# Optimization experiments

Measured on AMD Instinct MI355X. Metric: run time of the kernel, lower is better.

## Reference

```python
import jax, jax.numpy as jnp
import numpy as np

N_NODES = 100000
N_EDGES = 1600000
IN_F, HID_F, OUT_F = 128, 128, 64


def setup_inputs() -> dict:
    key = jax.random.key(0)
    ks = jax.random.split(key, 8)
    x = jax.random.normal(ks[0], (N_NODES, IN_F), dtype=jnp.float32)
    edge_index = jax.random.randint(ks[1], (2, N_EDGES), 0, N_NODES, dtype=jnp.int64)
    w1 = jax.random.normal(ks[2], (IN_F, HID_F), dtype=jnp.float32) * 0.05
    b1 = jax.random.normal(ks[3], (HID_F,), dtype=jnp.float32) * 0.05
    c1 = jax.random.normal(ks[4], (IN_F, HID_F, 3), dtype=jnp.float32) * 0.01
    w2 = jax.random.normal(ks[5], (HID_F, OUT_F), dtype=jnp.float32) * 0.05
    b2 = jax.random.normal(ks[6], (OUT_F,), dtype=jnp.float32) * 0.05
    c2 = jax.random.normal(ks[7], (IN_F, OUT_F, 3), dtype=jnp.float32) * 0.01
    return {"x": x, "edge_index": edge_index, "w1": w1, "b1": b1, "c1": c1,
            "w2": w2, "b2": b2, "c2": c2}


def _minimal_kan(x, w, b, c):
    # linear term: (N, out)
    lin = x @ w + b
    # polynomial basis (x, x^2, x^3): (N, in, 3)
    basis = jnp.stack([x, x * x, x * x * x], axis=-1)
    # fused contraction over (in, 3); same math as the (N,in,out,3) broadcast-sum
    kan_out = jnp.einsum('nib,iob->no', basis, c)
    return lin + 0.1 * kan_out


def _aggregate(h, source, target, num_nodes):
    # mean over incoming messages, degree clamped at 1
    deg = jax.ops.segment_sum(jnp.ones(source.shape[0], dtype=h.dtype), target,
                              num_segments=num_nodes)
    deg = jnp.maximum(deg, 1.0)
    out = jax.ops.segment_sum(h[source], target, num_segments=num_nodes)
    return out / deg[:, None]


def reference(x, edge_index, w1, b1, c1, w2, b2, c2):
    source, target = edge_index[0], edge_index[1]
    n = x.shape[0]
    h = _minimal_kan(x, w1, b1, c1)
    h = jax.nn.relu(h)
    h = _aggregate(h, source, target, n)
    h = _minimal_kan(h, w2, b2, c2)
    h = _aggregate(h, source, target, n)
    return jax.nn.log_softmax(h, axis=-1)
```

## Files before the change

### kernel.cpp

```cpp
#include <hip/hip_runtime.h>
#include <hip/hip_bf16.h>
#include <math.h>

#define N_NODES 100000
#define N_EDGES 1600000
#define IN_F 128
#define HID_F 128
#define OUT_F 64
#define K_TOT 384
#define BST 392

#define BK_BITS 9
#define BK_SIZE 512
#define NBUCK ((N_NODES + BK_SIZE - 1) / BK_SIZE)
#define EPB 4096
#define NBLK_SORT ((N_EDGES + EPB - 1) / EPB)
#define BCAP 10240
#define PCAP (BCAP + 7 * BK_SIZE)
#define PK_SRC_MASK 0x7fffffu
#define PAD8(d) (((d) + 7) & ~7)

typedef __attribute__((ext_vector_type(8))) short s8v;
typedef __attribute__((ext_vector_type(4))) short s4v;
typedef __attribute__((ext_vector_type(4))) float f4v;
typedef __attribute__((ext_vector_type(2))) float f2v;

__device__ __forceinline__ short f2bf(float f) {
    __hip_bfloat16 h = __float2bfloat16(f);
    return __builtin_bit_cast(short, h);
}

__global__ __launch_bounds__(256) void fold_weights_bf16(
    const float* __restrict__ w1, const float* __restrict__ c1,
    const float* __restrict__ w2, const float* __restrict__ c2,
    short* __restrict__ Wb1, short* __restrict__ Wb2,
    unsigned* __restrict__ h1d, unsigned* __restrict__ h2d,
    int* __restrict__ bcur)
{
    if (blockIdx.x == 0) {
        if (threadIdx.x < 32) h1d[(size_t)N_NODES * 32 + threadIdx.x] = 0;
        if (threadIdx.x < 16) h2d[(size_t)N_NODES * 16 + threadIdx.x] = 0;
        if (threadIdx.x < NBUCK) bcur[threadIdx.x] = threadIdx.x * BCAP;
    }
    int idx = blockIdx.x * 256 + threadIdx.x;
    if (idx < K_TOT * HID_F) {
        int k = idx >> 7, n = idx & 127;
        int p = k >> 7, f = k & 127;
        int si = f * HID_F + n;
        float v = (p == 0) ? (w1[si] + 0.1f * c1[si * 3])
                           : 0.1f * c1[si * 3 + p];
        Wb1[(((k >> 3) * HID_F) + n) * 8 + (k & 7)] = f2bf(v);
    } else {
        idx -= K_TOT * HID_F;
        if (idx < K_TOT * OUT_F) {
            int k = idx >> 6, n = idx & 63;
            int p = k >> 7, f = k & 127;
            int si = f * OUT_F + n;
            float v = (p == 0) ? (w2[si] + 0.1f * c2[si * 3])
                               : 0.1f * c2[si * 3 + p];
            Wb2[(((k >> 3) * OUT_F) + n) * 8 + (k & 7)] = f2bf(v);
        }
    }
}

__global__ __launch_bounds__(256) void scatter_kan1(
    const int* __restrict__ src, const int* __restrict__ tgt,
    int* __restrict__ bcur, unsigned* __restrict__ spk,
    const float* __restrict__ x, const short* __restrict__ Wb,
    const float* __restrict__ bias, unsigned* __restrict__ h1d)
{
    __shared__ __align__(16) char smem[64 * BST * 2];
    const int tid = threadIdx.x;

    if (blockIdx.x < NBLK_SORT) {
        int* h    = (int*)smem;
        int* base = h + NBUCK;
        int* tg   = base + NBUCK;
        for (int i = tid; i < NBUCK; i += 256) h[i] = 0;
        __syncthreads();
        int e0 = blockIdx.x * EPB;
        int n = min(EPB, N_EDGES - e0);
        for (int i = tid; i < n; i += 256) {
            int t = tgt[e0 + i];
            tg[i] = t;
            atomicAdd(&h[t >> BK_BITS], 1);
        }
        __syncthreads();
        for (int i = tid; i < NBUCK; i += 256) {
            int c = h[i];
            base[i] = c ? atomicAdd(&bcur[i], c) : 0;
            h[i] = 0;
        }
        __syncthreads();
        for (int i = tid; i < n; i += 256) {
            int t = tg[i];
            int b = t >> BK_BITS;
            int pos = base[b] + atomicAdd(&h[b], 1);
            spk[pos] = ((unsigned)(t - (b << BK_BITS)) << 23) | (unsigned)src[e0 + i];
        }
        return;
    }

    short* sb = (short*)smem;
    const int lane = tid & 63;
    const int wave = tid >> 6;
    const int node0 = (blockIdx.x - NBLK_SORT) * 64;
    const int q = lane >> 4, r = lane & 15;

#pragma unroll
    for (int it = 0; it < 8; ++it) {
        int idx = tid + 256 * it;
        int m = idx >> 5, c4 = (idx & 31) * 4;
        int gm = min(node0 + m, N_NODES - 1);
        float4 v = *(const float4*)(x + (size_t)gm * IN_F + c4);
        float vv[4] = {v.x, v.y, v.z, v.w};
        s4v p0, p1, p2;
#pragma unroll
        for (int t = 0; t < 4; ++t) {
            float e = vv[t], e2 = e * e, e3 = e2 * e;
            p0[t] = f2bf(e); p1[t] = f2bf(e2); p2[t] = f2bf(e3);
        }
        short* row = sb + m * BST + c4;
        *(s4v*)(row)       = p0;
        *(s4v*)(row + 128) = p1;
        *(s4v*)(row + 256) = p2;
    }
    __syncthreads();

    const int wm = (wave & 1) * 32;
    const int wn = (wave >> 1) * 64;

    f4v acc[2][4];
#pragma unroll
    for (int i = 0; i < 2; ++i)
#pragma unroll
        for (int j = 0; j < 4; ++j)
            acc[i][j] = (f4v){0.f, 0.f, 0.f, 0.f};

    float bj[4];
#pragma unroll
    for (int j = 0; j < 4; ++j) bj[j] = bias[wn + j * 16 + r];

#pragma unroll
    for (int kb = 0; kb < 12; ++kb) {
        const int col = kb * 32 + q * 8;
        s8v afrag[2];
#pragma unroll
        for (int i = 0; i < 2; ++i)
            afrag[i] = *(const s8v*)(sb + (wm + i * 16 + r) * BST + col);
#pragma unroll
        for (int j = 0; j < 4; ++j) {
            const s8v b = *(const s8v*)(Wb + (((kb * 4 + q) * HID_F) + wn + j * 16 + r) * 8);
            acc[0][j] = __builtin_amdgcn_mfma_f32_16x16x32_bf16(afrag[0], b, acc[0][j], 0, 0, 0);
            acc[1][j] = __builtin_amdgcn_mfma_f32_16x16x32_bf16(afrag[1], b, acc[1][j], 0, 0, 0);
        }
    }

    const int dci = ((wn >> 6) << 4) + r;
#pragma unroll
    for (int i = 0; i < 2; ++i)
#pragma unroll
        for (int e = 0; e < 4; ++e) {
            int grow = node0 + wm + i * 16 + q * 4 + e;
            if (grow < N_NODES) {
                float v0 = fmaxf(acc[i][0][e] + bj[0], 0.f);
                float v1 = fmaxf(acc[i][1][e] + bj[1], 0.f);
                float v2 = fmaxf(acc[i][2][e] + bj[2], 0.f);
                float v3 = fmaxf(acc[i][3][e] + bj[3], 0.f);
                int pk = __builtin_amdgcn_cvt_pk_fp8_f32(v0, v1, 0, false);
                pk = __builtin_amdgcn_cvt_pk_fp8_f32(v2, v3, pk, true);
                h1d[(size_t)grow * 32 + dci] = (unsigned)pk;
            }
        }
}

__global__ __launch_bounds__(512) void csr_build(
    const int* __restrict__ bcur, const unsigned* __restrict__ spk,
    int* __restrict__ deg, int* __restrict__ prow, int* __restrict__ csr_pad)
{
    __shared__ int d[BK_SIZE];
    __shared__ int pst[BK_SIZE];
    __shared__ int s[BK_SIZE];
    int tid = threadIdx.x;
    int b = blockIdx.x;
    d[tid] = 0;
    __syncthreads();
    int e0 = b * BCAP, e1 = bcur[b];
    for (int i = e0 + tid; i < e1; i += 512)
        atomicAdd(&d[spk[i] >> 23], 1);
    __syncthreads();
    int nbase = b << BK_BITS;
    int node = nbase + tid;
    int a = d[tid];
    if (node < N_NODES) deg[node] = a;
    int pc = (node < N_NODES) ? PAD8(a) : 0;
    s[tid] = pc;
    __syncthreads();
    for (int o = 1; o < 512; o <<= 1) {
        int t = (tid >= o) ? s[tid - o] : 0;
        __syncthreads();
        s[tid] += t;
        __syncthreads();
    }
    int excl = s[tid] - pc;
    int base = b * PCAP + excl;
    if (node < N_NODES) prow[node] = base;
    __syncthreads();
    d[tid] = base;
    pst[tid] = base + pc;
    __syncthreads();
    for (int i = e0 + tid; i < e1; i += 512) {
        unsigned pk = spk[i];
        int pos = atomicAdd(&d[pk >> 23], 1);
        csr_pad[pos] = (int)(pk & PK_SRC_MASK);
    }
    __syncthreads();
    {
        int kend = pst[tid];
        for (int k = d[tid]; k < kend; ++k) csr_pad[k] = N_NODES;
    }
}

__global__ __launch_bounds__(256) void gather128(
    const unsigned* __restrict__ h1d, const int* __restrict__ prow,
    const int* __restrict__ deg, const int* __restrict__ csr_pad,
    unsigned* __restrict__ a1d)
{
    const int lane  = threadIdx.x & 63;
    const int wave  = threadIdx.x >> 6;
    const int hl    = lane & 31;
    const int half  = lane >> 5;
    const int hbase = half << 5;
    const int node  = blockIdx.x * 8 + wave * 2 + half;

    int p0 = prow[node];
    int cnt = PAD8(deg[node]);
    int p1 = p0 + cnt;
    int cmax = max(cnt, __shfl_xor(cnt, 32));

    float acc[4][4];
#pragma unroll
    for (int t = 0; t < 4; ++t)
#pragma unroll
        for (int b = 0; b < 4; ++b) acc[t][b] = 0.f;

    for (int base = 0; base < cmax; base += 32) {
        int idx = max(min(p0 + base + hl, p1 - 1), 0);
        int sreg = csr_pad[idx];
        int lim = min(32, cmax - base);
        for (int j = 0; j < lim; j += 4) {
            if (base + j < cnt) {
                unsigned u[4];
#pragma unroll
                for (int t = 0; t < 4; ++t) {
                    int sj = __shfl(sreg, hbase + j + t);
                    u[t] = h1d[(size_t)sj * 32 + hl];
                }
#pragma unroll
                for (int t = 0; t < 4; ++t) {
                    f2v lo = __builtin_amdgcn_cvt_pk_f32_fp8(u[t], false);
                    f2v hi = __builtin_amdgcn_cvt_pk_f32_fp8(u[t], true);
                    acc[t][0] += lo.x; acc[t][1] += lo.y;
                    acc[t][2] += hi.x; acc[t][3] += hi.y;
                }
            }
        }
    }

    float s0 = (acc[0][0] + acc[1][0]) + (acc[2][0] + acc[3][0]);
    float s1 = (acc[0][1] + acc[1][1]) + (acc[2][1] + acc[3][1]);
    float s2 = (acc[0][2] + acc[1][2]) + (acc[2][2] + acc[3][2]);
    float s3 = (acc[0][3] + acc[1][3]) + (acc[2][3] + acc[3][3]);
    int pk = __builtin_amdgcn_cvt_pk_fp8_f32(s0, s1, 0, false);
    pk = __builtin_amdgcn_cvt_pk_fp8_f32(s2, s3, pk, true);
    a1d[(size_t)node * 32 + hl] = (unsigned)pk;
}

__global__ __launch_bounds__(256) void kan2_mfma(
    const unsigned* __restrict__ a1d, const int* __restrict__ deg,
    const short* __restrict__ Wb, const float* __restrict__ bias,
    unsigned short* __restrict__ h2s)
{
    __shared__ short sb[64 * BST];
    const int tid  = threadIdx.x;
    const int lane = tid & 63;
    const int wave = tid >> 6;
    const int node0 = blockIdx.x * 64;
    const int q = lane >> 4, r = lane & 15;

#pragma unroll
    for (int gi = 0; gi < 2; ++gi) {
        int g = tid + 256 * gi;
        int m = g >> 3, cg = (g & 7) * 4;
        int gm = min(node0 + m, N_NODES - 1);
        float di = 1.0f / fmaxf((float)deg[gm], 1.0f);
        uint4 u4 = *(const uint4*)(a1d + (size_t)gm * 32 + cg);
        unsigned uw[4] = {u4.x, u4.y, u4.z, u4.w};
        float xv[4][4];
#pragma unroll
        for (int j = 0; j < 4; ++j) {
            f2v lo = __builtin_amdgcn_cvt_pk_f32_fp8(uw[j], false);
            f2v hi = __builtin_amdgcn_cvt_pk_f32_fp8(uw[j], true);
            xv[j][0] = lo.x * di; xv[j][1] = lo.y * di;
            xv[j][2] = hi.x * di; xv[j][3] = hi.y * di;
        }
        int fb = ((cg >> 4) << 6) + (cg & 15);
#pragma unroll
        for (int b = 0; b < 4; ++b) {
            s4v p0, p1, p2;
#pragma unroll
            for (int j = 0; j < 4; ++j) {
                float e = xv[j][b], e2 = e * e, e3 = e2 * e;
                p0[j] = f2bf(e); p1[j] = f2bf(e2); p2[j] = f2bf(e3);
            }
            short* row = sb + m * BST + fb + 16 * b;
            *(s4v*)(row)       = p0;
            *(s4v*)(row + 128) = p1;
            *(s4v*)(row + 256) = p2;
        }
    }
    __syncthreads();

    const int wm = (wave & 1) * 32;
    const int wn = (wave >> 1) * 32;

    f4v acc[2][2];
#pragma unroll
    for (int i = 0; i < 2; ++i)
#pragma unroll
        for (int j = 0; j < 2; ++j)
            acc[i][j] = (f4v){0.f, 0.f, 0.f, 0.f};

    float bj[2];
#pragma unroll
    for (int j = 0; j < 2; ++j) bj[j] = bias[wn + j * 16 + r];

#pragma unroll
    for (int kb = 0; kb < 12; ++kb) {
        const int col = kb * 32 + q * 8;
        s8v afrag[2];
#pragma unroll
        for (int i = 0; i < 2; ++i)
            afrag[i] = *(const s8v*)(sb + (wm + i * 16 + r) * BST + col);
#pragma unroll
        for (int j = 0; j < 2; ++j) {
            const s8v b = *(const s8v*)(Wb + (((kb * 4 + q) * OUT_F) + wn + j * 16 + r) * 8);
            acc[0][j] = __builtin_amdgcn_mfma_f32_16x16x32_bf16(afrag[0], b, acc[0][j], 0, 0, 0);
            acc[1][j] = __builtin_amdgcn_mfma_f32_16x16x32_bf16(afrag[1], b, acc[1][j], 0, 0, 0);
        }
    }

    const int sslot = (wn >> 1) + r;
#pragma unroll
    for (int i = 0; i < 2; ++i)
#pragma unroll
        for (int e = 0; e < 4; ++e) {
            int grow = node0 + wm + i * 16 + q * 4 + e;
            if (grow < N_NODES) {
                float vlo = acc[i][0][e] + bj[0];
                float vhi = acc[i][1][e] + bj[1];
                int pk = __builtin_amdgcn_cvt_pk_fp8_f32(vlo, vhi, 0, false);
                h2s[(size_t)grow * 32 + sslot] = (unsigned short)(pk & 0xffff);
            }
        }
}

__global__ __launch_bounds__(256) void gather64_lsm(
    const unsigned short* __restrict__ h2s, const int* __restrict__ deg,
    const int* __restrict__ prow, const int* __restrict__ csr_pad,
    float* __restrict__ out)
{
    const int lane = threadIdx.x & 63;
    const int wave = threadIdx.x >> 6;
    const int hl   = lane & 31;
    const int half = lane >> 5;
    const int node = blockIdx.x * 8 + wave * 2 + half;

    int p0 = prow[node];
    int degr = deg[node];
    int cnt = PAD8(degr);
    int p1 = p0 + cnt;
    int cmax = max(cnt, __shfl_xor(cnt, 32));

    float alo[8], ahi[8];
#pragma unroll
    for (int t = 0; t < 8; ++t) { alo[t] = 0.f; ahi[t] = 0.f; }

    for (int base = 0; base < cmax; base += 32) {
        int idx = max(min(p0 + base + hl, p1 - 1), 0);
        int sreg = csr_pad[idx];
        int lim = min(32, cmax - base);
        for (int j = 0; j < lim; j += 8) {
            if (base + j < cnt) {
                int u[8];
#pragma unroll
                for (int t = 0; t < 8; ++t) {
                    int sj = __shfl(sreg, (half << 5) + j + t);
                    u[t] = (int)h2s[(size_t)sj * 32 + hl];
                }
#pragma unroll
                for (int t = 0; t < 8; ++t) {
                    alo[t] += __builtin_amdgcn_cvt_f32_fp8(u[t], 0);
                    ahi[t] += __builtin_amdgcn_cvt_f32_fp8(u[t], 1);
                }
            }
        }
    }
    float slo = ((alo[0] + alo[1]) + (alo[2] + alo[3])) + ((alo[4] + alo[5]) + (alo[6] + alo[7]));
    float shi = ((ahi[0] + ahi[1]) + (ahi[2] + ahi[3])) + ((ahi[4] + ahi[5]) + (ahi[6] + ahi[7]));

    float di = 1.0f / fmaxf((float)degr, 1.0f);
    float vlo = slo * di, vhi = shi * di;

    float m = fmaxf(vlo, vhi);
#pragma unroll
    for (int off = 16; off >= 1; off >>= 1)
        m = fmaxf(m, __shfl_xor(m, off));
    float e = expf(vlo - m) + expf(vhi - m);
#pragma unroll
    for (int off = 16; off >= 1; off >>= 1)
        e += __shfl_xor(e, off);
    float ls = logf(e);

    const int f_lo = ((hl >> 4) << 5) + (hl & 15);
    out[(size_t)node * OUT_F + f_lo]      = vlo - m - ls;
    out[(size_t)node * OUT_F + f_lo + 16] = vhi - m - ls;
}

extern "C" void kernel_launch(void* const* d_in, const int* in_sizes, int n_in,
                              void* d_out, int out_size, void* d_ws, size_t ws_size,
                              hipStream_t stream)
{
    const float* x  = (const float*)d_in[0];
    const int*   ei = (const int*)d_in[1];
    const float* w1 = (const float*)d_in[2];
    const float* b1 = (const float*)d_in[3];
    const float* c1 = (const float*)d_in[4];
    const float* w2 = (const float*)d_in[5];
    const float* b2 = (const float*)d_in[6];
    const float* c2 = (const float*)d_in[7];
    float* out = (float*)d_out;

    const int* src = ei;
    const int* tgt = ei + N_EDGES;

    char* ws = (char*)d_ws;
    size_t off = 0;
    auto carve = [&](size_t bytes) -> void* {
        void* p = ws + off;
        off = (off + bytes + 255) & ~(size_t)255;
        return p;
    };
    short*    Wb1       = (short*)carve((size_t)K_TOT * HID_F * 2);
    short*    Wb2       = (short*)carve((size_t)K_TOT * OUT_F * 2);
    int*      deg       = (int*)carve((size_t)N_NODES * 4);
    int*      prow      = (int*)carve((size_t)N_NODES * 4);
    int*      bcur      = (int*)carve((size_t)NBUCK * 4);
    unsigned* spk       = (unsigned*)carve((size_t)NBUCK * BCAP * 4);
    int*      csr_pad   = (int*)carve((size_t)NBUCK * PCAP * 4);
    unsigned* h1d       = (unsigned*)carve(((size_t)N_NODES + 1) * 128);
    unsigned* a1d       = (unsigned*)carve((size_t)N_NODES * 128);
    unsigned short* h2s = (unsigned short*)carve(((size_t)N_NODES + 1) * 64);

    const int grid_mm = (N_NODES + 63) / 64;

    fold_weights_bf16<<<(K_TOT * HID_F + K_TOT * OUT_F + 255) / 256, 256, 0, stream>>>(
        w1, c1, w2, c2, Wb1, Wb2, h1d, (unsigned*)h2s, bcur);

    scatter_kan1<<<NBLK_SORT + grid_mm, 256, 0, stream>>>(
        src, tgt, bcur, spk, x, Wb1, b1, h1d);

    csr_build<<<NBUCK, 512, 0, stream>>>(bcur, spk, deg, prow, csr_pad);

    gather128<<<(N_NODES + 7) / 8, 256, 0, stream>>>(h1d, prow, deg, csr_pad, a1d);

    kan2_mfma<<<grid_mm, 256, 0, stream>>>(a1d, deg, Wb2, b2, h2s);

    gather64_lsm<<<(N_NODES + 7) / 8, 256, 0, stream>>>(
        h2s, deg, prow, csr_pad, out);
}
```

Measured before the change: 231.2 us.

## Split KAN1 GEMM blocks across scatter and CSR-build launches to overlap phases

Moves the first KAN layer's per-node GEMM into a device function and splits its tiles between the edge-scatter kernel (first 781 tiles) and a merged CSR-build kernel (the remaining tiles). The idea is to fill idle compute during the latency-bound CSR build with independent matmul work. Buckets shrink from 512 to 256 nodes so the CSR build runs with 256-thread blocks and more blocks, which changes the packed key layout (24-bit source, 8-bit local index). This adds register and shared-memory pressure to the CSR kernel and relies on a fixed split constant.

```diff
diff --git a/kernel.cpp b/kernel.cpp
--- a/kernel.cpp
+++ b/kernel.cpp
@@ -10,15 +10,19 @@
 #define K_TOT 384
 #define BST 392
 
-#define BK_BITS 9
-#define BK_SIZE 512
+#define BK_BITS 8
+#define BK_SIZE 256
 #define NBUCK ((N_NODES + BK_SIZE - 1) / BK_SIZE)
 #define EPB 4096
 #define NBLK_SORT ((N_EDGES + EPB - 1) / EPB)
-#define BCAP 10240
+#define BCAP 5120
 #define PCAP (BCAP + 7 * BK_SIZE)
-#define PK_SRC_MASK 0x7fffffu
+#define PK_SRC_MASK 0xffffffu
 #define PAD8(d) (((d) + 7) & ~7)
+
+#define K1T ((N_NODES + 63) / 64)
+#define K1A 781
+#define K1B (K1T - K1A)
 
 typedef __attribute__((ext_vector_type(8))) short s8v;
 typedef __attribute__((ext_vector_type(4))) short s4v;
@@ -40,7 +44,7 @@
     if (blockIdx.x == 0) {
         if (threadIdx.x < 32) h1d[(size_t)N_NODES * 32 + threadIdx.x] = 0;
         if (threadIdx.x < 16) h2d[(size_t)N_NODES * 16 + threadIdx.x] = 0;
-        if (threadIdx.x < NBUCK) bcur[threadIdx.x] = threadIdx.x * BCAP;
+        for (int i = threadIdx.x; i < NBUCK; i += 256) bcur[i] = i * BCAP;
     }
     int idx = blockIdx.x * 256 + threadIdx.x;
     if (idx < K_TOT * HID_F) {
@@ -63,48 +67,14 @@
     }
 }
 
-__global__ __launch_bounds__(256) void scatter_kan1(
-    const int* __restrict__ src, const int* __restrict__ tgt,
-    int* __restrict__ bcur, unsigned* __restrict__ spk,
+__device__ __forceinline__ void kan1_body(
+    short* sb, int node0,
     const float* __restrict__ x, const short* __restrict__ Wb,
     const float* __restrict__ bias, unsigned* __restrict__ h1d)
 {
-    __shared__ __align__(16) char smem[64 * BST * 2];
-    const int tid = threadIdx.x;
-
-    if (blockIdx.x < NBLK_SORT) {
-        int* h    = (int*)smem;
-        int* base = h + NBUCK;
-        int* tg   = base + NBUCK;
-        for (int i = tid; i < NBUCK; i += 256) h[i] = 0;
-        __syncthreads();
-        int e0 = blockIdx.x * EPB;
-        int n = min(EPB, N_EDGES - e0);
-        for (int i = tid; i < n; i += 256) {
-            int t = tgt[e0 + i];
-            tg[i] = t;
-            atomicAdd(&h[t >> BK_BITS], 1);
-        }
-        __syncthreads();
-        for (int i = tid; i < NBUCK; i += 256) {
-            int c = h[i];
-            base[i] = c ? atomicAdd(&bcur[i], c) : 0;
-            h[i] = 0;
-        }
-        __syncthreads();
-        for (int i = tid; i < n; i += 256) {
-            int t = tg[i];
-            int b = t >> BK_BITS;
-            int pos = base[b] + atomicAdd(&h[b], 1);
-            spk[pos] = ((unsigned)(t - (b << BK_BITS)) << 23) | (unsigned)src[e0 + i];
-        }
-        return;
-    }
-
-    short* sb = (short*)smem;
+    const int tid  = threadIdx.x;
     const int lane = tid & 63;
     const int wave = tid >> 6;
-    const int node0 = (blockIdx.x - NBLK_SORT) * 64;
     const int q = lane >> 4, r = lane & 15;
 
 #pragma unroll
@@ -174,51 +144,101 @@
         }
 }
 
-__global__ __launch_bounds__(512) void csr_build(
+__global__ __launch_bounds__(256) void scatter_kan1(
+    const int* __restrict__ src, const int* __restrict__ tgt,
+    int* __restrict__ bcur, unsigned* __restrict__ spk,
+    const float* __restrict__ x, const short* __restrict__ Wb,
+    const float* __restrict__ bias, unsigned* __restrict__ h1d)
+{
+    __shared__ __align__(16) char smem[64 * BST * 2];
+    const int tid = threadIdx.x;
+
+    if (blockIdx.x < NBLK_SORT) {
+        int* h    = (int*)smem;
+        int* base = h + NBUCK;
+        int* tg   = base + NBUCK;
+        for (int i = tid; i < NBUCK; i += 256) h[i] = 0;
+        __syncthreads();
+        int e0 = blockIdx.x * EPB;
+        int n = min(EPB, N_EDGES - e0);
+        for (int i = tid; i < n; i += 256) {
+            int t = tgt[e0 + i];
+            tg[i] = t;
+            atomicAdd(&h[t >> BK_BITS], 1);
+        }
+        __syncthreads();
+        for (int i = tid; i < NBUCK; i += 256) {
+            int c = h[i];
+            base[i] = c ? atomicAdd(&bcur[i], c) : 0;
+            h[i] = 0;
+        }
+        __syncthreads();
+        for (int i = tid; i < n; i += 256) {
+            int t = tg[i];
+            int b = t >> BK_BITS;
+            int pos = base[b] + atomicAdd(&h[b], 1);
+            spk[pos] = ((unsigned)(t - (b << BK_BITS)) << 24) | (unsigned)src[e0 + i];
+        }
+        return;
+    }
+
+    kan1_body((short*)smem, ((int)blockIdx.x - NBLK_SORT) * 64, x, Wb, bias, h1d);
+}
+
+__global__ __launch_bounds__(256) void csr_kan1(
     const int* __restrict__ bcur, const unsigned* __restrict__ spk,
-    int* __restrict__ deg, int* __restrict__ prow, int* __restrict__ csr_pad)
-{
-    __shared__ int d[BK_SIZE];
-    __shared__ int pst[BK_SIZE];
-    __shared__ int s[BK_SIZE];
-    int tid = threadIdx.x;
-    int b = blockIdx.x;
-    d[tid] = 0;
-    __syncthreads();
-    int e0 = b * BCAP, e1 = bcur[b];
-    for (int i = e0 + tid; i < e1; i += 512)
-        atomicAdd(&d[spk[i] >> 23], 1);
-    __syncthreads();
-    int nbase = b << BK_BITS;
-    int node = nbase + tid;
-    int a = d[tid];
-    if (node < N_NODES) deg[node] = a;
-    int pc = (node < N_NODES) ? PAD8(a) : 0;
-    s[tid] = pc;
-    __syncthreads();
-    for (int o = 1; o < 512; o <<= 1) {
-        int t = (tid >= o) ? s[tid - o] : 0;
-        __syncthreads();
-        s[tid] += t;
-        __syncthreads();
-    }
-    int excl = s[tid] - pc;
-    int base = b * PCAP + excl;
-    if (node < N_NODES) prow[node] = base;
-    __syncthreads();
-    d[tid] = base;
-    pst[tid] = base + pc;
-    __syncthreads();
-    for (int i = e0 + tid; i < e1; i += 512) {
-        unsigned pk = spk[i];
-        int pos = atomicAdd(&d[pk >> 23], 1);
-        csr_pad[pos] = (int)(pk & PK_SRC_MASK);
-    }
-    __syncthreads();
-    {
-        int kend = pst[tid];
-        for (int k = d[tid]; k < kend; ++k) csr_pad[k] = N_NODES;
-    }
+    int* __restrict__ deg, int* __restrict__ prow, int* __restrict__ csr_pad,
+    const float* __restrict__ x, const short* __restrict__ Wb,
+    const float* __restrict__ bias, unsigned* __restrict__ h1d)
+{
+    __shared__ __align__(16) char smem[64 * BST * 2];
+    const int tid = threadIdx.x;
+
+    if (blockIdx.x < NBUCK) {
+        int* d   = (int*)smem;
+        int* pst = d + BK_SIZE;
+        int* s   = pst + BK_SIZE;
+        int b = blockIdx.x;
+        d[tid] = 0;
+        __syncthreads();
+        int e0 = b * BCAP, e1 = bcur[b];
+        for (int i = e0 + tid; i < e1; i += 256)
+            atomicAdd(&d[spk[i] >> 24], 1);
+        __syncthreads();
+        int nbase = b << BK_BITS;
+        int node = nbase + tid;
+        int a = d[tid];
+        if (node < N_NODES) deg[node] = a;
+        int pc = (node < N_NODES) ? PAD8(a) : 0;
+        s[tid] = pc;
+        __syncthreads();
+        for (int o = 1; o < 256; o <<= 1) {
+            int t = (tid >= o) ? s[tid - o] : 0;
+            __syncthreads();
+            s[tid] += t;
+            __syncthreads();
+        }
+        int excl = s[tid] - pc;
+        int base = b * PCAP + excl;
+        if (node < N_NODES) prow[node] = base;
+        __syncthreads();
+        d[tid] = base;
+        pst[tid] = base + pc;
+        __syncthreads();
+        for (int i = e0 + tid; i < e1; i += 256) {
+            unsigned pk = spk[i];
+            int pos = atomicAdd(&d[pk >> 24], 1);
+            csr_pad[pos] = (int)(pk & PK_SRC_MASK);
+        }
+        __syncthreads();
+        {
+            int kend = pst[tid];
+            for (int k = d[tid]; k < kend; ++k) csr_pad[k] = N_NODES;
+        }
+        return;
+    }
+
+    kan1_body((short*)smem, (K1A + (int)blockIdx.x - NBUCK) * 64, x, Wb, bias, h1d);
 }
 
 __global__ __launch_bounds__(256) void gather128(
@@ -462,19 +482,18 @@
     unsigned* a1d       = (unsigned*)carve((size_t)N_NODES * 128);
     unsigned short* h2s = (unsigned short*)carve(((size_t)N_NODES + 1) * 64);
 
-    const int grid_mm = (N_NODES + 63) / 64;
-
     fold_weights_bf16<<<(K_TOT * HID_F + K_TOT * OUT_F + 255) / 256, 256, 0, stream>>>(
         w1, c1, w2, c2, Wb1, Wb2, h1d, (unsigned*)h2s, bcur);
 
-    scatter_kan1<<<NBLK_SORT + grid_mm, 256, 0, stream>>>(
+    scatter_kan1<<<NBLK_SORT + K1A, 256, 0, stream>>>(
         src, tgt, bcur, spk, x, Wb1, b1, h1d);
 
-    csr_build<<<NBUCK, 512, 0, stream>>>(bcur, spk, deg, prow, csr_pad);
+    csr_kan1<<<NBUCK + K1B, 256, 0, stream>>>(
+        bcur, spk, deg, prow, csr_pad, x, Wb1, b1, h1d);
 
     gather128<<<(N_NODES + 7) / 8, 256, 0, stream>>>(h1d, prow, deg, csr_pad, a1d);
 
-    kan2_mfma<<<grid_mm, 256, 0, stream>>>(a1d, deg, Wb2, b2, h2s);
+    kan2_mfma<<<(N_NODES + 63) / 64, 256, 0, stream>>>(a1d, deg, Wb2, b2, h2s);
 
     gather64_lsm<<<(N_NODES + 7) / 8, 256, 0, stream>>>(
         h2s, deg, prow, csr_pad, out);
```

Result: no change. 230.9 us (-0.1%).
